# Optimization experiments

Hardware: AMD Instinct MI355X
Metric: run time of the kernel (lower is better)

The kernel has to match this reference:

```python
import jax, jax.numpy as jnp
import numpy as np
import math

N, E = 50000, 800000
DM, H, L = 128, 8, 6
D = DM // H  # per-head dim = 16
FF = 4 * DM
EPS = 1e-5


def _ln(x, g, b):
    mu = jnp.mean(x, axis=-1, keepdims=True)
    var = jnp.mean((x - mu) ** 2, axis=-1, keepdims=True)
    return (x - mu) * jax.lax.rsqrt(var + EPS) * g + b


def setup_inputs() -> dict:
    key = jax.random.key(0)
    ks = jax.random.split(key, 20)
    s = 0.05
    inp = {
        "node_features": jax.random.normal(ks[0], (N, 20), jnp.float32),
        "edge_attr": jax.random.normal(ks[1], (E, 3), jnp.float32),
        "edge_index": jax.random.randint(ks[2], (2, E), 0, N, jnp.int32),
        "emb_W": jax.random.normal(ks[3], (20, DM), jnp.float32) * s,
        "emb_b": jnp.zeros((DM,), jnp.float32),
        "Wq": jax.random.normal(ks[4], (L, DM, DM), jnp.float32) * s,
        "Wk": jax.random.normal(ks[5], (L, DM, DM), jnp.float32) * s,
        "Wv": jax.random.normal(ks[6], (L, DM, DM), jnp.float32) * s,
        "eW1": jax.random.normal(ks[7], (L, 3, D), jnp.float32) * s,
        "eb1": jnp.zeros((L, D), jnp.float32),
        "eW2": jax.random.normal(ks[8], (L, D, DM), jnp.float32) * s,
        "eb2": jnp.zeros((L, DM), jnp.float32),
        "ln_g": jnp.ones((L, DM), jnp.float32),
        "ln_b": jnp.zeros((L, DM), jnp.float32),
        "ff_W1": jax.random.normal(ks[9], (L, DM, FF), jnp.float32) * s,
        "ff_b1": jnp.zeros((L, FF), jnp.float32),
        "ff_W2": jax.random.normal(ks[10], (L, FF, DM), jnp.float32) * s,
        "ff_b2": jnp.zeros((L, DM), jnp.float32),
    }
    return inp


def reference(node_features, edge_attr, emb_W, emb_b, Wq, Wk, Wv,
              eW1, eb1, eW2, eb2, ln_g, ln_b, ff_W1, ff_b1, ff_W2, ff_b2,
              edge_index):
    src = edge_index[0]  # j: message source
    dst = edge_index[1]  # i: message target
    x = node_features @ emb_W + emb_b  # [N, DM]
    scale = 1.0 / math.sqrt(D)
    for l in range(L):
        q = (x @ Wq[l]).reshape(N, H, D)
        k = (x @ Wk[l]).reshape(N, H, D)
        v = (x @ Wv[l]).reshape(N, H, D)
        ee = (jnp.maximum(edge_attr @ eW1[l] + eb1[l], 0.0) @ eW2[l] + eb2[l]).reshape(E, H, D)
        # per-edge attention logits over heads (softmax over head axis, as in source)
        attn = jnp.einsum('ehd,ehd->eh', q[dst], k[src] + ee) * scale
        attn = jax.nn.softmax(attn, axis=1)  # [E, H]
        msg = (attn[..., None] * v[src]).reshape(E, H * D)  # per-head messages, concat heads
        agg = jax.ops.segment_sum(msg, dst, num_segments=N)  # scatter-add
        x = _ln(x + agg, ln_g[l], ln_b[l])
        h = jnp.maximum(x @ ff_W1[l] + ff_b1[l], 0.0) @ ff_W2[l] + ff_b2[l]
        x = _ln(x + h, ln_g[l], ln_b[l])  # same LN params reused, as in source
    return x
```

## Files before the change

kernel.cpp:

```cpp
#include <hip/hip_runtime.h>
#include <cstdint>
#include <cstddef>

#define NN 50000
#define NE 800000
#define NP 50048
#define ROWT 391
#define NBLK 196

typedef unsigned short u16;
typedef _Float16 f16;
typedef _Float16 hf8 __attribute__((ext_vector_type(8)));
typedef float f32x4 __attribute__((ext_vector_type(4)));

union U32 { unsigned u; f16 h[2]; };
union U64 { uint2 v; f16 h[4]; };
union U128 { uint4 v; f16 x[8]; };

__device__ __forceinline__ float b2f(u16 v){ return __uint_as_float((unsigned)v << 16); }
__device__ __forceinline__ u16 f2b(float f){
  unsigned u = __float_as_uint(f);
  return (u16)((u + 0x7fffu + ((u >> 16) & 1u)) >> 16);
}
__device__ __forceinline__ float ldf(const void* p, long i, int f32){
  return f32 ? ((const float*)p)[i] : b2f(((const u16*)p)[i]);
}
__device__ __forceinline__ void gl_lds16(const void* g, void* l){
  __builtin_amdgcn_global_load_lds((const __attribute__((address_space(1))) void*)g,
                                   (__attribute__((address_space(3))) void*)l, 16, 0, 0);
}

__global__ void detect_k(const u16* __restrict__ nf, int* __restrict__ flag)
{
  int mx = 0;
  for (int i = 0; i < 256; ++i) { int e = (nf[i] >> 7) & 0xFF; mx = e > mx ? e : mx; }
  flag[0] = (mx >= 0x90) ? 1 : 0;
}

__global__ void zero_i_k(int* __restrict__ p, int n)
{
  int i = blockIdx.x * 256 + threadIdx.x;
  if (i < n) p[i] = 0;
}

__global__ void conv_k(const void* eW1, const void* eb1, const void* eb2,
                       const void* lng, const void* lnb, const void* fb1, const void* fb2,
                       const void* embB, const void* embW,
                       float* __restrict__ pf, const int* __restrict__ dflag)
{
  int f32 = dflag[0];
  int i = blockIdx.x * 256 + threadIdx.x;
  if (i >= 9216) return;
  const void* p; long off;
  if (i < 288)       { p = eW1;  off = i; }
  else if (i < 384)  { p = eb1;  off = i - 288; }
  else if (i < 1152) { p = eb2;  off = i - 384; }
  else if (i < 1920) { p = lng;  off = i - 1152; }
  else if (i < 2688) { p = lnb;  off = i - 1920; }
  else if (i < 5760) { p = fb1;  off = i - 2688; }
  else if (i < 6528) { p = fb2;  off = i - 5760; }
  else if (i < 6656) { p = embB; off = i - 6528; }
  else               { p = embW; off = i - 6656; }
  pf[i] = ldf(p, off, f32);
}

__global__ void prep_qkve_k(const void* __restrict__ Wq, const void* __restrict__ Wk,
                            const void* __restrict__ Wv, const void* __restrict__ eW2,
                            f16* __restrict__ Wcat, const int* __restrict__ dflag)
{
  int f32 = dflag[0];
  int idx = blockIdx.x * 256 + threadIdx.x;
  int l = idx >> 16;
  int rem = idx & 65535;
  int r = rem >> 7;
  int kk = rem & 127;
  long base = (long)l * 16384;
  float val;
  if (r < 384) {
    const void* W = (r < 128) ? Wq : (r < 256) ? Wk : Wv;
    int n = r & 127;
    val = ldf(W, base + kk * 128 + n, f32);
  } else {
    int n = r - 384, h = n >> 4, j = n & 15;
    long wq = base + kk * 128 + h * 16;
    long e2 = (long)l * 2048 + j * 128 + h * 16;
    float s = 0.f;
    #pragma unroll
    for (int d = 0; d < 16; ++d) s += ldf(Wq, wq + d, f32) * ldf(eW2, e2 + d, f32);
    val = s;
  }
  Wcat[idx] = (f16)val;
}

__global__ void transpose_k(const void* __restrict__ in, f16* __restrict__ out, int R, int C,
                            const int* __restrict__ dflag)
{
  int f32 = dflag[0];
  int idx = blockIdx.x * 256 + threadIdx.x;
  int rc = R * C;
  int l = idx / rc, rem = idx % rc;
  int r = rem / C, c = rem % C;
  out[l * rc + c * R + r] = (f16)ldf(in, idx, f32);
}

__global__ void deg_count_k(const int* __restrict__ eidx, int* __restrict__ deg)
{
  int e = blockIdx.x * 256 + threadIdx.x;
  if (e < NE) atomicAdd(&deg[eidx[NE + e]], 1);
}

__global__ void scan_a(const int* __restrict__ deg, int* __restrict__ bsum)
{
  __shared__ int tmp[256];
  int t = threadIdx.x, i = blockIdx.x * 256 + t;
  int v = (i < NN) ? deg[i] : 0;
  tmp[t] = v; __syncthreads();
  for (int o = 1; o < 256; o <<= 1) {
    int u = (t >= o) ? tmp[t - o] : 0;
    __syncthreads(); tmp[t] += u; __syncthreads();
  }
  if (t == 255) bsum[blockIdx.x] = tmp[255];
}

__global__ void scan_b(const int* __restrict__ bsum, int* __restrict__ boff)
{
  __shared__ int tmp[256];
  int t = threadIdx.x;
  int v = (t < NBLK) ? bsum[t] : 0;
  tmp[t] = v; __syncthreads();
  for (int o = 1; o < 256; o <<= 1) {
    int u = (t >= o) ? tmp[t - o] : 0;
    __syncthreads(); tmp[t] += u; __syncthreads();
  }
  if (t < NBLK) boff[t] = tmp[t] - v;
}

__global__ void scan_c(const int* __restrict__ deg, const int* __restrict__ boff,
                       int* __restrict__ rstart, int* __restrict__ cursor)
{
  __shared__ int tmp[256];
  int t = threadIdx.x, i = blockIdx.x * 256 + t;
  int v = (i < NN) ? deg[i] : 0;
  tmp[t] = v; __syncthreads();
  for (int o = 1; o < 256; o <<= 1) {
    int u = (t >= o) ? tmp[t - o] : 0;
    __syncthreads(); tmp[t] += u; __syncthreads();
  }
  if (i <= NN) {
    int ex = boff[blockIdx.x] + tmp[t] - v;
    rstart[i] = ex;
    if (i < NN) cursor[i] = ex;
  }
}

__global__ void csr_fill_k(const int* __restrict__ eidx, int* __restrict__ cursor,
                           int* __restrict__ csrc, int* __restrict__ ceid)
{
  int e = blockIdx.x * 256 + threadIdx.x;
  if (e >= NE) return;
  int d = eidx[NE + e];
  int slot = atomicAdd(&cursor[d], 1);
  csrc[slot] = eidx[e];
  ceid[slot] = e;
}

__global__ void ea_gather_k(const void* __restrict__ eatt, const int* __restrict__ ceid,
                            f16* __restrict__ ea4, const int* __restrict__ dflag)
{
  int f32 = dflag[0];
  int e = blockIdx.x * 256 + threadIdx.x;
  if (e >= NE) return;
  long id = ceid[e];
  f16* q = ea4 + (size_t)e * 4;
  q[0] = (f16)ldf(eatt, id * 3 + 0, f32);
  q[1] = (f16)ldf(eatt, id * 3 + 1, f32);
  q[2] = (f16)ldf(eatt, id * 3 + 2, f32);
  q[3] = (f16)0.f;
}

__global__ void emb_k(const void* __restrict__ nf, const float* __restrict__ embWf,
                      const float* __restrict__ embBf, float* __restrict__ xf,
                      f16* __restrict__ xh, const int* __restrict__ dflag)
{
  int f32 = dflag[0];
  int idx = blockIdx.x * 256 + threadIdx.x;
  int node = idx >> 7, c = idx & 127;
  float s = 0.f;
  if (node < NN) {
    s = embBf[c];
    long row = (long)node * 20;
    #pragma unroll
    for (int f = 0; f < 20; ++f) s += ldf(nf, row + f, f32) * embWf[f * 128 + c];
  }
  xf[idx] = s;
  xh[idx] = (f16)s;
}

template<int MODE>
__global__ __launch_bounds__(256)
void gemm_k(const f16* __restrict__ A, const f16* __restrict__ Bt, int K,
            f16* __restrict__ o0, f16* __restrict__ o1, f16* __restrict__ o3,
            const float* __restrict__ bias)
{
  __shared__ __align__(16) f16 sh[128 * 136];
  f16* lA = sh;
  f16* lB = sh + 8192;
  const int tid = threadIdx.x;
  const int wave = tid >> 6, lane = tid & 63;
  const int wr = wave >> 1, wc = wave & 1;
  const size_t rowBase = (size_t)blockIdx.x * 128;
  const size_t colBase = (size_t)blockIdx.y * 128;
  const int m = lane & 15, q4 = lane >> 4;

  f32x4 zero = {0.f, 0.f, 0.f, 0.f};
  f32x4 acc[4][4];
  #pragma unroll
  for (int i = 0; i < 4; ++i)
    #pragma unroll
    for (int j = 0; j < 4; ++j) acc[i][j] = zero;

  const int sr = lane >> 3, sc = lane & 7;
  const f16* Ap = A + (rowBase + wave * 32 + sr) * (size_t)K + sc * 8;
  const f16* Bp = Bt + (colBase + wave * 32 + sr) * (size_t)K + sc * 8;
  f16* lAp = lA + wave * 2048;
  f16* lBp = lB + wave * 2048;

  for (int k0 = 0; k0 < K; k0 += 64) {
    #pragma unroll
    for (int i = 0; i < 4; ++i) {
      gl_lds16(Ap + k0 + (size_t)(8 * i) * K, lAp + i * 512);
      gl_lds16(Bp + k0 + (size_t)(8 * i) * K, lBp + i * 512);
    }
    __syncthreads();
    hf8 af[2][4], bf[2][4];
    #pragma unroll
    for (int s = 0; s < 2; ++s)
      #pragma unroll
      for (int i = 0; i < 4; ++i) {
        af[s][i] = *(const hf8*)(lA + (wr * 64 + i * 16 + m) * 64 + s * 32 + q4 * 8);
        bf[s][i] = *(const hf8*)(lB + (wc * 64 + i * 16 + m) * 64 + s * 32 + q4 * 8);
      }
    #pragma unroll
    for (int s = 0; s < 2; ++s)
      #pragma unroll
      for (int i = 0; i < 4; ++i)
        #pragma unroll
        for (int j = 0; j < 4; ++j)
          acc[i][j] = __builtin_amdgcn_mfma_f32_16x16x32_f16(bf[s][j], af[s][i], acc[i][j], 0, 0, 0);
    __syncthreads();
  }

  #pragma unroll
  for (int i = 0; i < 4; ++i) {
    int crow = wr * 64 + i * 16 + m;
    #pragma unroll
    for (int j = 0; j < 4; ++j) {
      int ccol = wc * 64 + j * 16 + q4 * 4;
      float v[4];
      #pragma unroll
      for (int r = 0; r < 4; ++r) v[r] = acc[i][j][r];
      if (MODE == 1) {
        float4 bv = *(const float4*)(bias + (int)colBase + ccol);
        v[0] = fmaxf(v[0] + bv.x, 0.f); v[1] = fmaxf(v[1] + bv.y, 0.f);
        v[2] = fmaxf(v[2] + bv.z, 0.f); v[3] = fmaxf(v[3] + bv.w, 0.f);
      } else if (MODE == 2) {
        float4 bv = *(const float4*)(bias + ccol);
        v[0] += bv.x; v[1] += bv.y; v[2] += bv.z; v[3] += bv.w;
      }
      U64 pk;
      #pragma unroll
      for (int r = 0; r < 4; ++r) pk.h[r] = (f16)v[r];
      *(uint2*)(sh + crow * 136 + ccol) = pk.v;
    }
  }
  __syncthreads();

  f16* o; size_t ld; int off;
  if (MODE == 0) {
    if (blockIdx.y == 0)      { o = o0; ld = 128; off = 0; }
    else if (blockIdx.y == 1) { o = o1; ld = 256; off = 0; }
    else if (blockIdx.y == 2) { o = o1; ld = 256; off = 128; }
    else                      { o = o3; ld = 128; off = 0; }
  } else if (MODE == 1) { o = o0; ld = 512; off = (int)colBase; }
  else                  { o = o0; ld = 128; off = 0; }
  {
    int row = tid >> 1, half = tid & 1;
    const f16* srcp = sh + row * 136 + half * 64;
    f16* dstp = o + (rowBase + row) * ld + off + half * 64;
    #pragma unroll
    for (int k = 0; k < 8; ++k)
      *(uint4*)(dstp + k * 8) = *(const uint4*)(srcp + k * 8);
  }
}

__global__ void fuse_k(const f16* __restrict__ qf, const f16* __restrict__ qef,
                       const f16* __restrict__ kv, const f16* __restrict__ ea4,
                       const int* __restrict__ rstart, const int* __restrict__ csrc,
                       const float* __restrict__ eW1f, const float* __restrict__ eb1f,
                       const float* __restrict__ eb2f,
                       const float* __restrict__ gf, const float* __restrict__ bpf,
                       float* __restrict__ xf, f16* __restrict__ xh)
{
  int wave = threadIdx.x >> 6, lane = threadIdx.x & 63;
  int node = blockIdx.x * 4 + wave;
  if (node >= NN) return;
  int sub = lane >> 4, l = lane & 15;
  int c0 = l << 3;
  int half = l & 1;
  size_t nb = (size_t)node * 128 + c0;

  float q[8], z[8];
  { U128 u; u.v = *(const uint4*)(qf + nb);
    #pragma unroll
    for (int i = 0; i < 8; ++i) q[i] = (float)u.x[i];
    u.v = *(const uint4*)(qef + nb);
    #pragma unroll
    for (int i = 0; i < 8; ++i) z[i] = (float)u.x[i]; }

  float pb = 0.f;
  #pragma unroll
  for (int i = 0; i < 8; ++i) pb = fmaf(q[i], eb2f[c0 + i], pb);
  pb += __shfl_xor(pb, 1);

  int j0 = half << 3;
  float w0[8], w1[8], w2[8], bb[8];
  #pragma unroll
  for (int i = 0; i < 8; ++i) {
    w0[i] = eW1f[j0 + i];
    w1[i] = eW1f[16 + j0 + i];
    w2[i] = eW1f[32 + j0 + i];
    bb[i] = eb1f[j0 + i];
  }

  float acc[8] = {0.f, 0.f, 0.f, 0.f, 0.f, 0.f, 0.f, 0.f};
  int e0 = rstart[node], e1 = rstart[node + 1];
  int e = e0 + sub;
  uint4 kN = {0,0,0,0}, vN = {0,0,0,0};
  uint2 eaN = {0,0};
  if (e < e1) {
    int s = csrc[e];
    const f16* kb = kv + (size_t)s * 256 + c0;
    kN = *(const uint4*)kb;
    vN = *(const uint4*)(kb + 128);
    eaN = *(const uint2*)(ea4 + (size_t)e * 4);
  }
  for (; e < e1; e += 4) {
    uint4 kC = kN, vC = vN; uint2 eaC = eaN;
    int en = e + 4;
    if (en < e1) {
      int s = csrc[en];
      const f16* kb = kv + (size_t)s * 256 + c0;
      kN = *(const uint4*)kb;
      vN = *(const uint4*)(kb + 128);
      eaN = *(const uint2*)(ea4 + (size_t)en * 4);
    }
    U64 ue; ue.v = eaC;
    float a0 = (float)ue.h[0], a1 = (float)ue.h[1], a2 = (float)ue.h[2];
    U128 K; K.v = kC;
    float p = 0.f;
    #pragma unroll
    for (int i = 0; i < 8; ++i) {
      float h = fmaxf(fmaf(a2, w2[i], fmaf(a1, w1[i], fmaf(a0, w0[i], bb[i]))), 0.f);
      p = fmaf(q[i], (float)K.x[i], fmaf(z[i], h, p));
    }
    p += __shfl_xor(p, 1);
    float logit = (p + pb) * 0.25f;
    float mx = logit;
    mx = fmaxf(mx, __shfl_xor(mx, 2));
    mx = fmaxf(mx, __shfl_xor(mx, 4));
    mx = fmaxf(mx, __shfl_xor(mx, 8));
    float ex = __expf(logit - mx);
    float se = ex;
    se += __shfl_xor(se, 2); se += __shfl_xor(se, 4); se += __shfl_xor(se, 8);
    float w = ex / se;
    U128 V; V.v = vC;
    #pragma unroll
    for (int i = 0; i < 8; ++i) acc[i] = fmaf(w, (float)V.x[i], acc[i]);
  }

  #pragma unroll
  for (int i = 0; i < 8; ++i) {
    acc[i] += __shfl_xor(acc[i], 16);
    acc[i] += __shfl_xor(acc[i], 32);
  }
  float4 x0 = *(const float4*)(xf + nb);
  float4 x1 = *(const float4*)(xf + nb + 4);
  float y[8] = { x0.x + acc[0], x0.y + acc[1], x0.z + acc[2], x0.w + acc[3],
                 x1.x + acc[4], x1.y + acc[5], x1.z + acc[6], x1.w + acc[7] };
  float s1 = 0.f, s2 = 0.f;
  #pragma unroll
  for (int i = 0; i < 8; ++i) { s1 += y[i]; s2 += y[i] * y[i]; }
  #pragma unroll
  for (int o = 1; o < 16; o <<= 1) { s1 += __shfl_xor(s1, o); s2 += __shfl_xor(s2, o); }
  float mu = s1 * 0.0078125f;
  float var = s2 * 0.0078125f - mu * mu;
  float rstd = rsqrtf(var + 1e-5f);
  float ov[8];
  #pragma unroll
  for (int i = 0; i < 8; ++i) ov[i] = (y[i] - mu) * rstd * gf[c0 + i] + bpf[c0 + i];
  if (sub == 0) {
    float4 s0 = { ov[0], ov[1], ov[2], ov[3] };
    float4 s1v = { ov[4], ov[5], ov[6], ov[7] };
    *(float4*)(xf + nb) = s0;
    *(float4*)(xf + nb + 4) = s1v;
    U128 wz;
    #pragma unroll
    for (int i = 0; i < 8; ++i) wz.x[i] = (f16)ov[i];
    *(uint4*)(xh + nb) = wz.v;
  }
}

__global__ void ln_res_k(const f16* __restrict__ add, float* __restrict__ xf,
                         f16* __restrict__ xh, const float* __restrict__ gf,
                         const float* __restrict__ bpf)
{
  int wave = threadIdx.x >> 6, lane = threadIdx.x & 63;
  int node = blockIdx.x * 4 + wave;
  if (node >= NN) return;
  int c0 = lane << 1;
  size_t nb = (size_t)node * 128 + c0;
  U32 ua; ua.u = *(const unsigned*)(add + nb);
  float y0 = xf[nb] + (float)ua.h[0];
  float y1 = xf[nb + 1] + (float)ua.h[1];
  float s1 = y0 + y1, s2 = y0 * y0 + y1 * y1;
  #pragma unroll
  for (int o = 1; o < 64; o <<= 1) { s1 += __shfl_xor(s1, o); s2 += __shfl_xor(s2, o); }
  float mu = s1 * 0.0078125f;
  float var = s2 * 0.0078125f - mu * mu;
  float rstd = rsqrtf(var + 1e-5f);
  float o0v = (y0 - mu) * rstd * gf[c0] + bpf[c0];
  float o1v = (y1 - mu) * rstd * gf[c0 + 1] + bpf[c0 + 1];
  xf[nb] = o0v; xf[nb + 1] = o1v;
  U32 wz; wz.h[0] = (f16)o0v; wz.h[1] = (f16)o1v;
  *(unsigned*)(xh + nb) = wz.u;
}

__global__ void out_k(const float* __restrict__ xf, void* __restrict__ out,
                      const int* __restrict__ dflag)
{
  int f32 = dflag[0];
  int idx = blockIdx.x * 256 + threadIdx.x;
  if (f32) ((float*)out)[idx] = xf[idx];
  else     ((u16*)out)[idx] = f2b(xf[idx]);
}

extern "C" void kernel_launch(void* const* d_in, const int* in_sizes, int n_in,
                              void* d_out, int out_size, void* d_ws, size_t ws_size,
                              hipStream_t stream)
{
  const void* nf   = d_in[0];
  const void* eatt = d_in[1];
  const int*  eidx = (const int*)d_in[2];
  const void* embW = d_in[3];
  const void* embB = d_in[4];
  const void* Wq   = d_in[5];
  const void* Wk   = d_in[6];
  const void* Wv   = d_in[7];
  const void* eW1  = d_in[8];
  const void* eb1  = d_in[9];
  const void* eW2  = d_in[10];
  const void* eb2  = d_in[11];
  const void* lng  = d_in[12];
  const void* lnb  = d_in[13];
  const void* fW1  = d_in[14];
  const void* fb1  = d_in[15];
  const void* fW2  = d_in[16];
  const void* fb2  = d_in[17];

  char* p = (char*)d_ws;
  auto alloc = [&](size_t b) { char* r = p; p += (b + 255) & ~(size_t)255; return r; };
  int* dflag   = (int*)alloc(256);
  float* pf    = (float*)alloc(9216 * 4);
  float* xf    = (float*)alloc((size_t)NP * 128 * 4);
  f16*   xh    = (f16*)  alloc((size_t)NP * 128 * 2);
  int* deg     = (int*)alloc((NN + 1) * 4);
  int* rst     = (int*)alloc((NN + 1) * 4);
  int* cur     = (int*)alloc((size_t)NN * 4);
  int* bsum    = (int*)alloc(NBLK * 4);
  int* boff    = (int*)alloc(NBLK * 4);
  int* csrc    = (int*)alloc((size_t)NE * 4);
  f16* ea4     = (f16*)alloc((size_t)NE * 4 * 2);
  f16* Wcat    = (f16*)alloc((size_t)6 * 512 * 128 * 2);
  f16* W1t     = (f16*)alloc((size_t)6 * 512 * 128 * 2);
  f16* W2t     = (f16*)alloc((size_t)6 * 128 * 512 * 2);
  char* S    = alloc((size_t)NP * 512 * 2 + (size_t)NP * 128 * 2);
  f16* qf  = (f16*)S;
  f16* qe  = qf + (size_t)NP * 128;
  f16* kv  = qe + (size_t)NP * 128;
  f16* hb  = (f16*)S;
  f16* ffh = hb + (size_t)NP * 512;
  int* ceid = (int*)S;

  float* eW1f = pf;
  float* eb1f = pf + 288;
  float* eb2f = pf + 384;
  float* lngf = pf + 1152;
  float* lnbf = pf + 1920;
  float* fb1f = pf + 2688;
  float* fb2f = pf + 5760;
  float* embBf = pf + 6528;
  float* embWf = pf + 6656;

  detect_k<<<1, 1, 0, stream>>>((const u16*)nf, dflag);
  conv_k<<<36, 256, 0, stream>>>(eW1, eb1, eb2, lng, lnb, fb1, fb2, embB, embW, pf, dflag);
  prep_qkve_k<<<1536, 256, 0, stream>>>(Wq, Wk, Wv, eW2, Wcat, dflag);
  transpose_k<<<1536, 256, 0, stream>>>(fW1, W1t, 128, 512, dflag);
  transpose_k<<<1536, 256, 0, stream>>>(fW2, W2t, 512, 128, dflag);
  zero_i_k<<<(NN + 256) / 256, 256, 0, stream>>>(deg, NN + 1);
  deg_count_k<<<3125, 256, 0, stream>>>(eidx, deg);
  scan_a<<<NBLK, 256, 0, stream>>>(deg, bsum);
  scan_b<<<1, 256, 0, stream>>>(bsum, boff);
  scan_c<<<NBLK, 256, 0, stream>>>(deg, boff, rst, cur);
  csr_fill_k<<<3125, 256, 0, stream>>>(eidx, cur, csrc, ceid);
  ea_gather_k<<<3125, 256, 0, stream>>>(eatt, ceid, ea4, dflag);
  emb_k<<<NP * 128 / 256, 256, 0, stream>>>(nf, embWf, embBf, xf, xh, dflag);

  for (int l = 0; l < 6; ++l) {
    gemm_k<0><<<dim3(ROWT, 4), 256, 0, stream>>>(xh, Wcat + (size_t)l * 65536, 128,
                                                 qf, kv, qe, nullptr);
    fuse_k<<<12500, 256, 0, stream>>>(qf, qe, kv, ea4, rst, csrc,
                                      eW1f + l * 48, eb1f + l * 16, eb2f + l * 128,
                                      lngf + l * 128, lnbf + l * 128, xf, xh);
    gemm_k<1><<<dim3(ROWT, 4), 256, 0, stream>>>(xh, W1t + (size_t)l * 65536, 128,
                                                 hb, nullptr, nullptr, fb1f + l * 512);
    gemm_k<2><<<dim3(ROWT, 1), 256, 0, stream>>>(hb, W2t + (size_t)l * 65536, 512,
                                                 ffh, nullptr, nullptr, fb2f + l * 128);
    ln_res_k<<<12500, 256, 0, stream>>>(ffh, xf, xh, lngf + l * 128, lnbf + l * 128);
  }
  out_k<<<25000, 256, 0, stream>>>(xf, d_out, dflag);
}
```

Measured before the change: 1.428 ms.

## Fuse residual LayerNorm into FFN second GEMM epilogue and deepen K tile

```diff
diff --git a/kernel.cpp b/kernel.cpp
--- a/kernel.cpp
+++ b/kernel.cpp
@@ -200,11 +200,13 @@
 __global__ __launch_bounds__(256)
 void gemm_k(const f16* __restrict__ A, const f16* __restrict__ Bt, int K,
             f16* __restrict__ o0, f16* __restrict__ o1, f16* __restrict__ o3,
-            const float* __restrict__ bias)
-{
-  __shared__ __align__(16) f16 sh[128 * 136];
+            const float* __restrict__ bias,
+            const float* __restrict__ gf, const float* __restrict__ bpf,
+            float* __restrict__ xf, f16* __restrict__ xh)
+{
+  __shared__ __align__(16) f16 sh[128 * 256];
   f16* lA = sh;
-  f16* lB = sh + 8192;
+  f16* lB = sh + 16384;
   const int tid = threadIdx.x;
   const int wave = tid >> 6, lane = tid & 63;
   const int wr = wave >> 1, wc = wave & 1;
@@ -219,34 +221,33 @@
     #pragma unroll
     for (int j = 0; j < 4; ++j) acc[i][j] = zero;
 
-  const int sr = lane >> 3, sc = lane & 7;
-  const f16* Ap = A + (rowBase + wave * 32 + sr) * (size_t)K + sc * 8;
-  const f16* Bp = Bt + (colBase + wave * 32 + sr) * (size_t)K + sc * 8;
-  f16* lAp = lA + wave * 2048;
-  f16* lBp = lB + wave * 2048;
-
-  for (int k0 = 0; k0 < K; k0 += 64) {
-    #pragma unroll
-    for (int i = 0; i < 4; ++i) {
-      gl_lds16(Ap + k0 + (size_t)(8 * i) * K, lAp + i * 512);
-      gl_lds16(Bp + k0 + (size_t)(8 * i) * K, lBp + i * 512);
+  const int sr4 = lane >> 4, sc16 = lane & 15;
+  const f16* Ap = A + (rowBase + wave * 32 + sr4) * (size_t)K + sc16 * 8;
+  const f16* Bp = Bt + (colBase + wave * 32 + sr4) * (size_t)K + sc16 * 8;
+  f16* lAp = lA + wave * 4096;
+  f16* lBp = lB + wave * 4096;
+
+  for (int k0 = 0; k0 < K; k0 += 128) {
+    #pragma unroll
+    for (int i = 0; i < 8; ++i) {
+      gl_lds16(Ap + k0 + (size_t)(4 * i) * K, lAp + i * 512);
+      gl_lds16(Bp + k0 + (size_t)(4 * i) * K, lBp + i * 512);
     }
     __syncthreads();
-    hf8 af[2][4], bf[2][4];
-    #pragma unroll
-    for (int s = 0; s < 2; ++s)
+    #pragma unroll
+    for (int kk = 0; kk < 4; ++kk) {
+      hf8 af[4], bf[4];
       #pragma unroll
       for (int i = 0; i < 4; ++i) {
-        af[s][i] = *(const hf8*)(lA + (wr * 64 + i * 16 + m) * 64 + s * 32 + q4 * 8);
-        bf[s][i] = *(const hf8*)(lB + (wc * 64 + i * 16 + m) * 64 + s * 32 + q4 * 8);
+        af[i] = *(const hf8*)(lA + (wr * 64 + i * 16 + m) * 128 + kk * 32 + q4 * 8);
+        bf[i] = *(const hf8*)(lB + (wc * 64 + i * 16 + m) * 128 + kk * 32 + q4 * 8);
       }
-    #pragma unroll
-    for (int s = 0; s < 2; ++s)
       #pragma unroll
       for (int i = 0; i < 4; ++i)
         #pragma unroll
         for (int j = 0; j < 4; ++j)
-          acc[i][j] = __builtin_amdgcn_mfma_f32_16x16x32_f16(bf[s][j], af[s][i], acc[i][j], 0, 0, 0);
+          acc[i][j] = __builtin_amdgcn_mfma_f32_16x16x32_f16(bf[j], af[i], acc[i][j], 0, 0, 0);
+    }
     __syncthreads();
   }
 
@@ -275,21 +276,60 @@
   }
   __syncthreads();
 
-  f16* o; size_t ld; int off;
-  if (MODE == 0) {
-    if (blockIdx.y == 0)      { o = o0; ld = 128; off = 0; }
-    else if (blockIdx.y == 1) { o = o1; ld = 256; off = 0; }
-    else if (blockIdx.y == 2) { o = o1; ld = 256; off = 128; }
-    else                      { o = o3; ld = 128; off = 0; }
-  } else if (MODE == 1) { o = o0; ld = 512; off = (int)colBase; }
-  else                  { o = o0; ld = 128; off = 0; }
-  {
+  if (MODE != 2) {
+    f16* o; size_t ld; int off;
+    if (MODE == 0) {
+      if (blockIdx.y == 0)      { o = o0; ld = 128; off = 0; }
+      else if (blockIdx.y == 1) { o = o1; ld = 256; off = 0; }
+      else if (blockIdx.y == 2) { o = o1; ld = 256; off = 128; }
+      else                      { o = o3; ld = 128; off = 0; }
+    } else { o = o0; ld = 512; off = (int)colBase; }
     int row = tid >> 1, half = tid & 1;
     const f16* srcp = sh + row * 136 + half * 64;
     f16* dstp = o + (rowBase + row) * ld + off + half * 64;
     #pragma unroll
     for (int k = 0; k < 8; ++k)
       *(uint4*)(dstp + k * 8) = *(const uint4*)(srcp + k * 8);
+  } else {
+    int row = tid >> 1, half = tid & 1;
+    size_t nb = (rowBase + row) * (size_t)128 + half * 64;
+    const f16* srcp = sh + row * 136 + half * 64;
+    float y[64];
+    float s1 = 0.f, s2 = 0.f;
+    #pragma unroll
+    for (int k = 0; k < 8; ++k) {
+      U128 u; u.v = *(const uint4*)(srcp + k * 8);
+      float4 xa = *(const float4*)(xf + nb + k * 8);
+      float4 xb = *(const float4*)(xf + nb + k * 8 + 4);
+      float xr[8] = { xa.x, xa.y, xa.z, xa.w, xb.x, xb.y, xb.z, xb.w };
+      #pragma unroll
+      for (int d = 0; d < 8; ++d) {
+        float t = (float)u.x[d] + xr[d];
+        y[k * 8 + d] = t; s1 += t; s2 += t * t;
+      }
+    }
+    s1 += __shfl_xor(s1, 1); s2 += __shfl_xor(s2, 1);
+    float mu = s1 * 0.0078125f;
+    float var = s2 * 0.0078125f - mu * mu;
+    float rstd = rsqrtf(var + 1e-5f);
+    int cb = half * 64;
+    #pragma unroll
+    for (int k = 0; k < 8; ++k) {
+      float4 oa, ob; U128 pk;
+      #pragma unroll
+      for (int d = 0; d < 4; ++d) {
+        float ov = (y[k * 8 + d] - mu) * rstd * gf[cb + k * 8 + d] + bpf[cb + k * 8 + d];
+        (&oa.x)[d] = ov; pk.x[d] = (f16)ov;
+      }
+      #pragma unroll
+      for (int d = 0; d < 4; ++d) {
+        float ov = (y[k * 8 + 4 + d] - mu) * rstd * gf[cb + k * 8 + 4 + d] + bpf[cb + k * 8 + 4 + d];
+        (&ob.x)[d] = ov; pk.x[4 + d] = (f16)ov;
+      }
+      *(float4*)(xf + nb + k * 8) = oa;
+      *(float4*)(xf + nb + k * 8 + 4) = ob;
+      *(uint4*)(xh + nb + k * 8) = pk.v;
+    }
   }
 }
 
@@ -408,31 +448,6 @@
     for (int i = 0; i < 8; ++i) wz.x[i] = (f16)ov[i];
     *(uint4*)(xh + nb) = wz.v;
   }
-}
-
-__global__ void ln_res_k(const f16* __restrict__ add, float* __restrict__ xf,
-                         f16* __restrict__ xh, const float* __restrict__ gf,
-                         const float* __restrict__ bpf)
-{
-  int wave = threadIdx.x >> 6, lane = threadIdx.x & 63;
-  int node = blockIdx.x * 4 + wave;
-  if (node >= NN) return;
-  int c0 = lane << 1;
-  size_t nb = (size_t)node * 128 + c0;
-  U32 ua; ua.u = *(const unsigned*)(add + nb);
-  float y0 = xf[nb] + (float)ua.h[0];
-  float y1 = xf[nb + 1] + (float)ua.h[1];
-  float s1 = y0 + y1, s2 = y0 * y0 + y1 * y1;
-  #pragma unroll
-  for (int o = 1; o < 64; o <<= 1) { s1 += __shfl_xor(s1, o); s2 += __shfl_xor(s2, o); }
-  float mu = s1 * 0.0078125f;
-  float var = s2 * 0.0078125f - mu * mu;
-  float rstd = rsqrtf(var + 1e-5f);
-  float o0v = (y0 - mu) * rstd * gf[c0] + bpf[c0];
-  float o1v = (y1 - mu) * rstd * gf[c0 + 1] + bpf[c0 + 1];
-  xf[nb] = o0v; xf[nb + 1] = o1v;
-  U32 wz; wz.h[0] = (f16)o0v; wz.h[1] = (f16)o1v;
-  *(unsigned*)(xh + nb) = wz.u;
 }
 
 __global__ void out_k(const float* __restrict__ xf, void* __restrict__ out,
@@ -488,7 +503,6 @@
   f16* qe  = qf + (size_t)NP * 128;
   f16* kv  = qe + (size_t)NP * 128;
   f16* hb  = (f16*)S;
-  f16* ffh = hb + (size_t)NP * 512;
   int* ceid = (int*)S;
 
   float* eW1f = pf;
@@ -517,15 +531,17 @@
 
   for (int l = 0; l < 6; ++l) {
     gemm_k<0><<<dim3(ROWT, 4), 256, 0, stream>>>(xh, Wcat + (size_t)l * 65536, 128,
-                                                 qf, kv, qe, nullptr);
+                                                 qf, kv, qe, nullptr,
+                                                 nullptr, nullptr, nullptr, nullptr);
     fuse_k<<<12500, 256, 0, stream>>>(qf, qe, kv, ea4, rst, csrc,
                                       eW1f + l * 48, eb1f + l * 16, eb2f + l * 128,
                                       lngf + l * 128, lnbf + l * 128, xf, xh);
     gemm_k<1><<<dim3(ROWT, 4), 256, 0, stream>>>(xh, W1t + (size_t)l * 65536, 128,
-                                                 hb, nullptr, nullptr, fb1f + l * 512);
+                                                 hb, nullptr, nullptr, fb1f + l * 512,
+                                                 nullptr, nullptr, nullptr, nullptr);
     gemm_k<2><<<dim3(ROWT, 1), 256, 0, stream>>>(hb, W2t + (size_t)l * 65536, 512,
-                                                 ffh, nullptr, nullptr, fb2f + l * 128);
-    ln_res_k<<<12500, 256, 0, stream>>>(ffh, xf, xh, lngf + l * 128, lnbf + l * 128);
+                                                 nullptr, nullptr, nullptr, fb2f + l * 128,
+                                                 lngf + l * 128, lnbf + l * 128, xf, xh);
   }
   out_k<<<25000, 256, 0, stream>>>(xf, d_out, dflag);
 }
```

Measured after the change: 1.539 ms. 7.7% more time.
